# Kernel tuning notes

Measured on AMD Instinct MI355X. Metric: run time of the kernel, lower is better.

Reference implementation:

```python
import jax, jax.numpy as jnp
import numpy as np

TRUNC = (26, 26, 26)
OUT = (32, 32, 32)


def _dct_mat(N):
    # Orthonormal DCT-II matrix, matching the torch loop construction.
    k = np.arange(N)[:, None].astype(np.float64)
    n = np.arange(N)[None, :].astype(np.float64)
    m = np.sqrt(2.0 / N) * np.cos(np.pi * (2.0 * n + 1.0) * k / (2.0 * N))
    m[0, :] = 1.0 / np.sqrt(N)
    return jnp.asarray(m, dtype=jnp.float32)


def setup_inputs() -> dict:
    key = jax.random.key(0)
    x = jax.random.normal(key, (8, 32, 64, 64, 64), dtype=jnp.float32)
    return {"x": x}


def reference(x):
    # x: (B, C, D, H, W) with D == H == W (required by the original permute+matmul chain)
    B, C, D, H, W = x.shape
    assert D == H == W, "SpectralPooling's matmul chain requires a cubic volume"
    M = _dct_mat(D)  # one matrix since cubic; dct_mat_depth==height==width

    y = x.astype(jnp.float32)
    for _ in range(3):
        y = jnp.matmul(M, jnp.transpose(y, (0, 1, 4, 3, 2)))
    y = jnp.transpose(y, (0, 1, 4, 3, 2))

    # Truncate low frequencies, zero-pad up to output_size.
    t = y[:, :, :TRUNC[0], :TRUNC[1], :TRUNC[2]]
    t = jnp.pad(
        t,
        ((0, 0), (0, 0),
         (0, OUT[0] - TRUNC[0]),
         (0, OUT[1] - TRUNC[1]),
         (0, OUT[2] - TRUNC[2])),
    )

    # Inverse 3D DCT (IDCT matrix = transpose of orthonormal DCT matrix).
    Mi = _dct_mat(OUT[0]).T
    for _ in range(3):
        t = jnp.matmul(Mi, jnp.transpose(t, (0, 1, 4, 3, 2)))
    return jnp.transpose(t, (0, 1, 4, 3, 2))  # (B, C, 32, 32, 32)
```

## Files before the change

### kernel.cpp

```cpp
#include <hip/hip_runtime.h>

#define PI_F 3.14159265358979323846f

#define FMA4S(acc, a, b)                  \
    acc.x = fmaf(a, b.x, acc.x);          \
    acc.y = fmaf(a, b.y, acc.y);          \
    acc.z = fmaf(a, b.z, acc.z);          \
    acc.w = fmaf(a, b.w, acc.w)

__global__ __launch_bounds__(1024) void build_C_kernel(float* __restrict__ Cout) {
    __shared__ __align__(16) float sM[64 * 64];
    __shared__ __align__(16) float s32a[32 * 32];
    __shared__ __align__(16) float s32b[32 * 32];
    __shared__ __align__(16) float s32c[32 * 32];
    __shared__ __align__(16) float sW[32 * 64];
    __shared__ __align__(16) float sW2[32 * 64];
    const int t = threadIdx.x;

    for (int i = t; i < 4096; i += 1024) {
        int k = i >> 6, n = i & 63;
        int m = ((2 * n + 1) * k) & 255;
        float v = (k == 0) ? 0.125f
                           : 0.17677669529663688f
                             * cosf(PI_F * (float)m / 128.0f);
        sM[i] = v;
    }
    {
        int k = t >> 5, n = t & 31;
        int m = ((2 * n + 1) * k) & 127;
        float v = (k == 0) ? 0.17677669529663688f
                           : 0.25f
                             * cosf(PI_F * (float)m / 64.0f);
        s32a[t] = v;
    }
    __syncthreads();

    if (t < 256) {
        int r = t >> 3, q = t & 7;
        float4 acc = make_float4(0.f, 0.f, 0.f, 0.f);
#pragma unroll 8
        for (int k = 0; k < 32; ++k) {
            float a = s32a[r * 32 + k];
            float4 b = *(const float4*)&s32a[k * 32 + q * 4];
            FMA4S(acc, a, b);
        }
        *(float4*)&s32b[r * 32 + q * 4] = acc;
    }
    __syncthreads();

    if (t < 256) {
        int r = t >> 3, q = t & 7;
        float4 acc = make_float4(0.f, 0.f, 0.f, 0.f);
#pragma unroll 8
        for (int k = 0; k < 32; ++k) {
            float a = s32b[r * 32 + k];
            float4 b = *(const float4*)&s32a[k * 32 + q * 4];
            FMA4S(acc, a, b);
        }
        *(float4*)&s32c[r * 32 + q * 4] = acc;
    }
    __syncthreads();

    if (t < 512) {
        int r = t >> 4, q = t & 15;
        float4 acc = make_float4(0.f, 0.f, 0.f, 0.f);
#pragma unroll 13
        for (int h1 = 0; h1 < 26; ++h1) {
            float a = s32c[h1 * 32 + r];
            float4 b = *(const float4*)&sM[h1 * 64 + q * 4];
            FMA4S(acc, a, b);
        }
        *(float4*)&sW[r * 64 + q * 4] = acc;
    }
    __syncthreads();

    if (t < 512) {
        int r = t >> 4, q = t & 15;
        float4 acc = make_float4(0.f, 0.f, 0.f, 0.f);
#pragma unroll 4
        for (int k4 = 0; k4 < 64; k4 += 4) {
            float4 a4 = *(const float4*)&sW[r * 64 + k4];
            float4 b0 = *(const float4*)&sM[(k4 + 0) * 64 + q * 4];
            float4 b1 = *(const float4*)&sM[(k4 + 1) * 64 + q * 4];
            float4 b2 = *(const float4*)&sM[(k4 + 2) * 64 + q * 4];
            float4 b3 = *(const float4*)&sM[(k4 + 3) * 64 + q * 4];
            FMA4S(acc, a4.x, b0);
            FMA4S(acc, a4.y, b1);
            FMA4S(acc, a4.z, b2);
            FMA4S(acc, a4.w, b3);
        }
        *(float4*)&sW2[r * 64 + q * 4] = acc;
    }
    __syncthreads();

    if (t < 512) {
        int r = t >> 4, q = t & 15;
        float4 acc = make_float4(0.f, 0.f, 0.f, 0.f);
#pragma unroll 4
        for (int k4 = 0; k4 < 64; k4 += 4) {
            float4 a4 = *(const float4*)&sW2[r * 64 + k4];
            float4 b0 = *(const float4*)&sM[(k4 + 0) * 64 + q * 4];
            float4 b1 = *(const float4*)&sM[(k4 + 1) * 64 + q * 4];
            float4 b2 = *(const float4*)&sM[(k4 + 2) * 64 + q * 4];
            float4 b3 = *(const float4*)&sM[(k4 + 3) * 64 + q * 4];
            FMA4S(acc, a4.x, b0);
            FMA4S(acc, a4.y, b1);
            FMA4S(acc, a4.z, b2);
            FMA4S(acc, a4.w, b3);
        }
        *(float4*)&Cout[r * 64 + q * 4] = acc;
    }
}

#define FMA4(a, c, xv)                    \
    a.x = fmaf(c, xv.x, a.x);             \
    a.y = fmaf(c, xv.y, a.y);             \
    a.z = fmaf(c, xv.z, a.z);             \
    a.w = fmaf(c, xv.w, a.w)

__global__ __launch_bounds__(256) void spectral_pool_kernel(
    const float* __restrict__ x, const float* __restrict__ C,
    float* __restrict__ out) {
    __shared__ __align__(16) float sC[32 * 68];
    __shared__ __align__(16) float xs[4][64 * 32];

    const int t   = threadIdx.x;
    const int blk = blockIdx.x;
    const int bc  = blk >> 3;
    const int dg  = blk & 7;
    const int s   = t >> 6;
    const int l   = t & 63;
    const int wq  = l & 7;
    const int hb  = l >> 3;
    const int d   = dg * 4 + s;

    const bool active = (d < 26);
    if (active) {
        const float* xp = x + (size_t)(bc * 64 + d) * 4096;
#pragma unroll
        for (int it = 0; it < 8; ++it) {
            int idx = it * 64 + l;
            int row = idx >> 3, q = idx & 7;
            const float* g = xp + row * 64 + q * 4;
            __builtin_amdgcn_global_load_lds(
                (const __attribute__((address_space(1))) void*)g,
                (__attribute__((address_space(3))) void*)(&xs[s][it * 256]),
                16, 0, 0);
        }
    }

    if (dg != 7) {
        {
            const float4* cg = (const float4*)(C + t * 8);
            float4 g0 = cg[0], g1 = cg[1];
            float* dst = sC + (t >> 3) * 68 + (t & 7) * 8;
            *(float4*)(dst)     = g0;
            *(float4*)(dst + 4) = g1;
        }
        __syncthreads();
    }

    float* op = out + (size_t)(bc * 32 + d) * 1024;

    if (!active) {
        const float4 z = make_float4(0.f, 0.f, 0.f, 0.f);
#pragma unroll
        for (int j = 0; j < 4; ++j)
            *(float4*)(op + (j * 64 + l) * 4) = z;
        return;
    }

    const float* xss = xs[s] + wq * 4;
    const float* cp  = sC + hb * 68;

    float4 a0 = make_float4(0.f, 0.f, 0.f, 0.f);
    float4 a1 = a0, a2 = a0, a3 = a0;

#pragma unroll 4
    for (int k4 = 0; k4 < 64; k4 += 4) {
        const float4 c0 = *(const float4*)(cp + k4);
        const float4 c1 = *(const float4*)(cp + 8 * 68 + k4);
        const float4 c2 = *(const float4*)(cp + 16 * 68 + k4);
        const float4 c3 = *(const float4*)(cp + 24 * 68 + k4);
        const float4 x0 = *(const float4*)(xss + (k4 + 0) * 32);
        const float4 x1 = *(const float4*)(xss + (k4 + 1) * 32);
        const float4 x2 = *(const float4*)(xss + (k4 + 2) * 32);
        const float4 x3 = *(const float4*)(xss + (k4 + 3) * 32);

        FMA4(a0, c0.x, x0); FMA4(a0, c0.y, x1); FMA4(a0, c0.z, x2); FMA4(a0, c0.w, x3);
        FMA4(a1, c1.x, x0); FMA4(a1, c1.y, x1); FMA4(a1, c1.z, x2); FMA4(a1, c1.w, x3);
        FMA4(a2, c2.x, x0); FMA4(a2, c2.y, x1); FMA4(a2, c2.z, x2); FMA4(a2, c2.w, x3);
        FMA4(a3, c3.x, x0); FMA4(a3, c3.y, x1); FMA4(a3, c3.z, x2); FMA4(a3, c3.w, x3);
    }

    const int w0 = wq * 4;
    if (w0 >= 26) {
        a0 = a1 = a2 = a3 = make_float4(0.f, 0.f, 0.f, 0.f);
    } else if (w0 == 24) {
        a0.z = a0.w = 0.f; a1.z = a1.w = 0.f;
        a2.z = a2.w = 0.f; a3.z = a3.w = 0.f;
    }

    *(float4*)(op + hb * 32 + w0)        = a0;
    *(float4*)(op + (hb + 8) * 32 + w0)  = a1;
    *(float4*)(op + (hb + 16) * 32 + w0) = a2;
    *(float4*)(op + (hb + 24) * 32 + w0) = a3;
}

extern "C" void kernel_launch(void* const* d_in, const int* in_sizes, int n_in,
                              void* d_out, int out_size, void* d_ws, size_t ws_size,
                              hipStream_t stream) {
    const float* x = (const float*)d_in[0];
    float* out = (float*)d_out;
    float* C = (float*)d_ws;

    hipLaunchKernelGGL(build_C_kernel, dim3(1), dim3(1024), 0, stream, C);
    hipLaunchKernelGGL(spectral_pool_kernel, dim3(2048), dim3(256), 0, stream,
                       x, C, out);
}
```

Baseline: 320.7 us.

## Double-buffer depth slices per block with async LDS loads, fewer blocks

Each block now handles 13 depth slices of one (b,c) pair, loading them in four rounds into double-buffered LDS with global_load_lds and explicit vmcnt waits, so the load of the next round overlaps compute on the current one. The grid shrinks from 2048 to 512 blocks, and the combined matrix C is loaded into shared memory once per block instead of once per 4 slices. C now lives in a device global instead of the workspace. The cost is a larger LDS footprint (64KB of x buffers plus C), which lowers occupancy, and correctness depends on the hand-written vmcnt counts.

```diff
diff --git a/kernel.cpp b/kernel.cpp
--- a/kernel.cpp
+++ b/kernel.cpp
@@ -1,6 +1,8 @@
 #include <hip/hip_runtime.h>
 
 #define PI_F 3.14159265358979323846f
+
+__device__ __align__(16) float g_C[32 * 64];
 
 #define FMA4S(acc, a, b)                  \
     acc.x = fmaf(a, b.x, acc.x);          \
@@ -8,7 +10,7 @@
     acc.z = fmaf(a, b.z, acc.z);          \
     acc.w = fmaf(a, b.w, acc.w)
 
-__global__ __launch_bounds__(1024) void build_C_kernel(float* __restrict__ Cout) {
+__global__ __launch_bounds__(1024) void build_C_kernel() {
     __shared__ __align__(16) float sM[64 * 64];
     __shared__ __align__(16) float s32a[32 * 32];
     __shared__ __align__(16) float s32b[32 * 32];
@@ -21,16 +23,14 @@
         int k = i >> 6, n = i & 63;
         int m = ((2 * n + 1) * k) & 255;
         float v = (k == 0) ? 0.125f
-                           : 0.17677669529663688f
-                             * cosf(PI_F * (float)m / 128.0f);
+                           : 0.17677669529663688f * cosf(PI_F * (float)m / 128.0f);
         sM[i] = v;
     }
     {
         int k = t >> 5, n = t & 31;
         int m = ((2 * n + 1) * k) & 127;
         float v = (k == 0) ? 0.17677669529663688f
-                           : 0.25f
-                             * cosf(PI_F * (float)m / 64.0f);
+                           : 0.25f * cosf(PI_F * (float)m / 64.0f);
         s32a[t] = v;
     }
     __syncthreads();
@@ -108,7 +108,7 @@
             FMA4S(acc, a4.z, b2);
             FMA4S(acc, a4.w, b3);
         }
-        *(float4*)&Cout[r * 64 + q * 4] = acc;
+        *(float4*)&g_C[r * 64 + q * 4] = acc;
     }
 }
 
@@ -119,92 +119,109 @@
     a.w = fmaf(c, xv.w, a.w)
 
 __global__ __launch_bounds__(256) void spectral_pool_kernel(
-    const float* __restrict__ x, const float* __restrict__ C,
-    float* __restrict__ out) {
+    const float* __restrict__ x, float* __restrict__ out) {
     __shared__ __align__(16) float sC[32 * 68];
-    __shared__ __align__(16) float xs[4][64 * 32];
-
-    const int t   = threadIdx.x;
-    const int blk = blockIdx.x;
-    const int bc  = blk >> 3;
-    const int dg  = blk & 7;
-    const int s   = t >> 6;
-    const int l   = t & 63;
-    const int wq  = l & 7;
-    const int hb  = l >> 3;
-    const int d   = dg * 4 + s;
-
-    const bool active = (d < 26);
-    if (active) {
-        const float* xp = x + (size_t)(bc * 64 + d) * 4096;
+    __shared__ __align__(16) float xs[2][4][64 * 32];
+
+    const int t     = threadIdx.x;
+    const int bc    = blockIdx.x >> 1;
+    const int half  = blockIdx.x & 1;
+    const int s     = t >> 6;
+    const int l     = t & 63;
+    const int wq    = l & 7;
+    const int hb    = l >> 3;
+    const int dbase = half * 13;
+
+    auto stage = [&](int buf, int r) {
+        int sl = r * 4 + s;
+        if (sl < 13) {
+            const float* xp = x + (size_t)(bc * 64 + dbase + sl) * 4096;
 #pragma unroll
-        for (int it = 0; it < 8; ++it) {
-            int idx = it * 64 + l;
-            int row = idx >> 3, q = idx & 7;
-            const float* g = xp + row * 64 + q * 4;
-            __builtin_amdgcn_global_load_lds(
-                (const __attribute__((address_space(1))) void*)g,
-                (__attribute__((address_space(3))) void*)(&xs[s][it * 256]),
-                16, 0, 0);
-        }
-    }
-
-    if (dg != 7) {
-        {
-            const float4* cg = (const float4*)(C + t * 8);
-            float4 g0 = cg[0], g1 = cg[1];
-            float* dst = sC + (t >> 3) * 68 + (t & 7) * 8;
-            *(float4*)(dst)     = g0;
-            *(float4*)(dst + 4) = g1;
-        }
-        __syncthreads();
-    }
-
-    float* op = out + (size_t)(bc * 32 + d) * 1024;
-
-    if (!active) {
+            for (int it = 0; it < 8; ++it) {
+                int idx = it * 64 + l;
+                int row = idx >> 3, q = idx & 7;
+                const float* g = xp + row * 64 + q * 4;
+                __builtin_amdgcn_global_load_lds(
+                    (const __attribute__((address_space(1))) void*)g,
+                    (__attribute__((address_space(3))) void*)(&xs[buf][s][it * 256]),
+                    16, 0, 0);
+            }
+        }
+    };
+
+    stage(0, 0);
+
+    {
+        const float4* cg = (const float4*)(g_C + t * 8);
+        float4 g0 = cg[0], g1 = cg[1];
+        float* dst = sC + (t >> 3) * 68 + (t & 7) * 8;
+        *(float4*)(dst)     = g0;
+        *(float4*)(dst + 4) = g1;
+    }
+    __syncthreads();
+
+#pragma unroll
+    for (int r = 0; r < 4; ++r) {
+        if (r < 3) stage((r + 1) & 1, r + 1);
+
+        if (r == 0) {
+        } else if (r < 3) {
+            asm volatile("s_waitcnt vmcnt(12)" ::: "memory");
+        } else {
+            asm volatile("s_waitcnt vmcnt(4)" ::: "memory");
+        }
+        __builtin_amdgcn_sched_barrier(0);
+
+        const int sl = r * 4 + s;
+        if (sl < 13) {
+            const int d = dbase + sl;
+            const float* xss = xs[r & 1][s] + wq * 4;
+            const float* cp  = sC + hb * 68;
+
+            float4 a0 = make_float4(0.f, 0.f, 0.f, 0.f);
+            float4 a1 = a0, a2 = a0, a3 = a0;
+
+#pragma unroll 4
+            for (int k4 = 0; k4 < 64; k4 += 4) {
+                const float4 c0 = *(const float4*)(cp + k4);
+                const float4 c1 = *(const float4*)(cp + 8 * 68 + k4);
+                const float4 c2 = *(const float4*)(cp + 16 * 68 + k4);
+                const float4 c3 = *(const float4*)(cp + 24 * 68 + k4);
+                const float4 x0 = *(const float4*)(xss + (k4 + 0) * 32);
+                const float4 x1 = *(const float4*)(xss + (k4 + 1) * 32);
+                const float4 x2 = *(const float4*)(xss + (k4 + 2) * 32);
+                const float4 x3 = *(const float4*)(xss + (k4 + 3) * 32);
+
+                FMA4(a0, c0.x, x0); FMA4(a0, c0.y, x1); FMA4(a0, c0.z, x2); FMA4(a0, c0.w, x3);
+                FMA4(a1, c1.x, x0); FMA4(a1, c1.y, x1); FMA4(a1, c1.z, x2); FMA4(a1, c1.w, x3);
+                FMA4(a2, c2.x, x0); FMA4(a2, c2.y, x1); FMA4(a2, c2.z, x2); FMA4(a2, c2.w, x3);
+                FMA4(a3, c3.x, x0); FMA4(a3, c3.y, x1); FMA4(a3, c3.z, x2); FMA4(a3, c3.w, x3);
+            }
+
+            const int w0 = wq * 4;
+            if (w0 >= 26) {
+                a0 = a1 = a2 = a3 = make_float4(0.f, 0.f, 0.f, 0.f);
+            } else if (w0 == 24) {
+                a0.z = a0.w = 0.f; a1.z = a1.w = 0.f;
+                a2.z = a2.w = 0.f; a3.z = a3.w = 0.f;
+            }
+
+            float* op = out + (size_t)(bc * 32 + d) * 1024;
+            *(float4*)(op + hb * 32 + w0)        = a0;
+            *(float4*)(op + (hb + 8) * 32 + w0)  = a1;
+            *(float4*)(op + (hb + 16) * 32 + w0) = a2;
+            *(float4*)(op + (hb + 24) * 32 + w0) = a3;
+        }
+    }
+
+    if (s < 3) {
+        const int zd = 26 + half * 3 + s;
+        float* op = out + (size_t)(bc * 32 + zd) * 1024;
         const float4 z = make_float4(0.f, 0.f, 0.f, 0.f);
 #pragma unroll
         for (int j = 0; j < 4; ++j)
             *(float4*)(op + (j * 64 + l) * 4) = z;
-        return;
-    }
-
-    const float* xss = xs[s] + wq * 4;
-    const float* cp  = sC + hb * 68;
-
-    float4 a0 = make_float4(0.f, 0.f, 0.f, 0.f);
-    float4 a1 = a0, a2 = a0, a3 = a0;
-
-#pragma unroll 4
-    for (int k4 = 0; k4 < 64; k4 += 4) {
-        const float4 c0 = *(const float4*)(cp + k4);
-        const float4 c1 = *(const float4*)(cp + 8 * 68 + k4);
-        const float4 c2 = *(const float4*)(cp + 16 * 68 + k4);
-        const float4 c3 = *(const float4*)(cp + 24 * 68 + k4);
-        const float4 x0 = *(const float4*)(xss + (k4 + 0) * 32);
-        const float4 x1 = *(const float4*)(xss + (k4 + 1) * 32);
-        const float4 x2 = *(const float4*)(xss + (k4 + 2) * 32);
-        const float4 x3 = *(const float4*)(xss + (k4 + 3) * 32);
-
-        FMA4(a0, c0.x, x0); FMA4(a0, c0.y, x1); FMA4(a0, c0.z, x2); FMA4(a0, c0.w, x3);
-        FMA4(a1, c1.x, x0); FMA4(a1, c1.y, x1); FMA4(a1, c1.z, x2); FMA4(a1, c1.w, x3);
-        FMA4(a2, c2.x, x0); FMA4(a2, c2.y, x1); FMA4(a2, c2.z, x2); FMA4(a2, c2.w, x3);
-        FMA4(a3, c3.x, x0); FMA4(a3, c3.y, x1); FMA4(a3, c3.z, x2); FMA4(a3, c3.w, x3);
-    }
-
-    const int w0 = wq * 4;
-    if (w0 >= 26) {
-        a0 = a1 = a2 = a3 = make_float4(0.f, 0.f, 0.f, 0.f);
-    } else if (w0 == 24) {
-        a0.z = a0.w = 0.f; a1.z = a1.w = 0.f;
-        a2.z = a2.w = 0.f; a3.z = a3.w = 0.f;
-    }
-
-    *(float4*)(op + hb * 32 + w0)        = a0;
-    *(float4*)(op + (hb + 8) * 32 + w0)  = a1;
-    *(float4*)(op + (hb + 16) * 32 + w0) = a2;
-    *(float4*)(op + (hb + 24) * 32 + w0) = a3;
+    }
 }
 
 extern "C" void kernel_launch(void* const* d_in, const int* in_sizes, int n_in,
@@ -212,9 +229,9 @@
                               hipStream_t stream) {
     const float* x = (const float*)d_in[0];
     float* out = (float*)d_out;
-    float* C = (float*)d_ws;
-
-    hipLaunchKernelGGL(build_C_kernel, dim3(1), dim3(1024), 0, stream, C);
-    hipLaunchKernelGGL(spectral_pool_kernel, dim3(2048), dim3(256), 0, stream,
-                       x, C, out);
+    (void)d_ws; (void)ws_size;
+
+    hipLaunchKernelGGL(build_C_kernel, dim3(1), dim3(1024), 0, stream);
+    hipLaunchKernelGGL(spectral_pool_kernel, dim3(512), dim3(256), 0, stream,
+                       x, out);
 }
```

Measured after the change: 323.0 us. About the same (+0.7%).
